# Kernel tuning notes

Hardware: AMD Instinct MI355X
Metric: run time of the kernel (lower is better)

The kernel has to match this reference:

```python
import jax, jax.numpy as jnp
import numpy as np

DIM = 512
NUM_HEADS = 8
HEAD_DIM = DIM // NUM_HEADS
SEGMENT_LENGTHS = (1024, 2048, 4096)
DILATED_RATIOS = (1, 2, 4)
SCALE = HEAD_DIM ** -0.5
NEG_FILL = -100000000.0  # matches torch masked_fill value


def setup_inputs() -> dict:
    key = jax.random.key(0)
    ks = jax.random.split(key, 8)
    b, L = 2, 8192
    def nrm(k, shape, s=1.0):
        return jax.random.normal(k, shape, dtype=jnp.float32) * s
    return {
        "query": nrm(ks[0], (b, L, DIM)),
        "key_": nrm(ks[1], (b, L, DIM)),
        "value": nrm(ks[2], (b, L, DIM)),
        "Wq": nrm(ks[3], (DIM, DIM), DIM ** -0.5),
        "Wk": nrm(ks[4], (DIM, DIM), DIM ** -0.5),
        "Wv": nrm(ks[5], (DIM, DIM), DIM ** -0.5),
        "Wo": nrm(ks[6], (DIM, DIM), DIM ** -0.5),
        "bo": nrm(ks[7], (DIM,), 0.01),
    }


def _branch(q, k, v, sl, dr):
    """One (segment_length, dilation) branch.
    q,k,v: (b, L, H, D). Returns dense out (b, L, H, D) and lse (b, L, H),
    with uncovered positions set to (0, NEG_FILL).
    gathering/dense_to_sparse reduces, per head hd, to selecting positions
    l*dr + (hd // (H//dr)) within each segment (diagonal of the r1 x r2 block).
    """
    b, L, H, D = q.shape
    n = L // sl          # segments per sequence
    hsub = H // dr       # heads per dilation offset
    lsub = sl // dr      # kept tokens per segment
    # (lsub, H): dilated position of each kept token for each head
    pos = jnp.arange(lsub)[:, None] * dr + (jnp.arange(H) // hsub)[None, :]
    hid = jnp.arange(H)[None, :]

    def gather(x):
        xs = x.reshape(b, n, sl, H, D)
        g = xs[:, :, pos, hid, :]                  # (b, n, lsub, H, D)
        return jnp.transpose(g, (0, 1, 3, 2, 4))    # (b, n, H, lsub, D)

    qi = gather(q) * SCALE
    ki = gather(k)
    vi = gather(v)
    scores = jnp.einsum('bnhld,bnhmd->bnhlm', qi, ki)
    lse = jax.nn.logsumexp(scores, axis=-1)                                  # (b, n, H, lsub)
    p = jax.nn.softmax(scores.astype(jnp.float32), axis=-1).astype(scores.dtype)
    o = jnp.einsum('bnhlm,bnhmd->bnhld', p, vi)                              # (b, n, H, lsub, D)
    # sparse_to_dense: scatter back onto dilated positions (diag_embed)
    o_ = jnp.transpose(o, (0, 1, 3, 2, 4))                                    # (b, n, lsub, H, D)
    od = jnp.zeros((b, n, sl, H, D), o.dtype).at[:, :, pos, hid, :].set(o_)
    ld = jnp.zeros((b, n, sl, H), lse.dtype).at[:, :, pos, hid].set(
        jnp.transpose(lse, (0, 1, 3, 2)))
    ld = jnp.where(ld == 0, NEG_FILL, ld)  # masked_fill_(lse == 0, -1e8)
    return od.reshape(b, L, H, D), ld.reshape(b, L, H)


def reference(query, key_, value, Wq, Wk, Wv, Wo, bo):
    b, L, _ = query.shape
    def heads(x, W):
        return (x @ W.T).reshape(b, L, NUM_HEADS, HEAD_DIM)
    q = heads(query, Wq)
    k = heads(key_, Wk)
    v = heads(value, Wv)
    outs, lses = [], []
    for sl, dr in zip(SEGMENT_LENGTHS, DILATED_RATIOS):
        o, l = _branch(q, k, v, sl, dr)
        outs.append(o)
        lses.append(l)
    # merge branches via logsumexp-weighted combination (weights detached in torch)
    lse_stack = jnp.stack(lses, 0)            # (nb, b, L, H)
    m = lse_stack.max(0)
    w = jnp.exp(lse_stack - m)
    w = w / w.sum(0)
    w = jax.lax.stop_gradient(w)
    out = sum(o * wi[..., None] for o, wi in zip(outs, list(w)))
    out = out.reshape(b, L, DIM)
    return out @ Wo.T + bo
```

## Files before the change

### kernel.cpp

```cpp
#include <hip/hip_runtime.h>
#include <hip/hip_bf16.h>

typedef unsigned short u16;
typedef unsigned int u32;
typedef __attribute__((ext_vector_type(8))) short short8;
typedef __attribute__((ext_vector_type(4))) float floatx4;
typedef __attribute__((ext_vector_type(2))) unsigned int uint2v;

__device__ __forceinline__ float b2f(u16 u) {
    u32 x = ((u32)u) << 16;
    return __builtin_bit_cast(float, x);
}
__device__ __forceinline__ u16 f2b(float f) {
    u32 x = __builtin_bit_cast(u32, f);
    return (u16)((x + 0x7fffu + ((x >> 16) & 1u)) >> 16);
}
__device__ __forceinline__ u32 pack2(float lo, float hi) {
    float2 f; f.x = lo; f.y = hi;
    __hip_bfloat162 h = __float22bfloat162_rn(f);
    u32 r;
    __builtin_memcpy(&r, &h, 4);
    return r;
}
__device__ __forceinline__ float fexp2(float x) {
#if __has_builtin(__builtin_amdgcn_exp2f)
    return __builtin_amdgcn_exp2f(x);
#else
    return __expf(x * 0.6931471805599453f);
#endif
}

__device__ __forceinline__ uint2v pl32(u32 a, u32 b) {
    return __builtin_amdgcn_permlane32_swap(a, b, false, false);
}

template<bool AF32>
__global__ __launch_bounds__(256) void gemm_bt_bias(
    const void* __restrict__ Ap, const float* __restrict__ B,
    u16* __restrict__ Cb, float* __restrict__ Cf, const float* __restrict__ bias,
    int M, int N, int K, float scale)
{
    __shared__ __align__(16) u16 a_lds[128][72];
    __shared__ __align__(16) u16 b_lds[128][72];
    const int tid = threadIdx.x;
    const int lane = tid & 63, wv = tid >> 6;
    const int quad = lane >> 4, l15 = lane & 15;
    const int tm = blockIdx.x, tn = blockIdx.y;
    const int wm = (wv >> 1) * 64, wn = (wv & 1) * 64;
    (void)M;

    floatx4 acc[4][4];
#pragma unroll
    for (int i = 0; i < 4; ++i)
#pragma unroll
        for (int j = 0; j < 4; ++j) acc[i][j] = (floatx4)0.f;

    for (int k0 = 0; k0 < K; k0 += 64) {
#pragma unroll
        for (int r = 0; r < 4; ++r) {
            int idx = r * 256 + tid;
            int row = idx >> 3, ch = (idx & 7) * 8;
            if constexpr (AF32) {
                const float* A = (const float*)Ap;
                const float* src = A + (size_t)(tm * 128 + row) * K + k0 + ch;
                float4 f0 = *(const float4*)src;
                float4 f1 = *(const float4*)(src + 4);
                uint4 pk;
                pk.x = pack2(f0.x, f0.y);
                pk.y = pack2(f0.z, f0.w);
                pk.z = pack2(f1.x, f1.y);
                pk.w = pack2(f1.z, f1.w);
                *(uint4*)&a_lds[row][ch] = pk;
            } else {
                const u16* A = (const u16*)Ap;
                *(uint4*)&a_lds[row][ch] =
                    *(const uint4*)(A + (size_t)(tm * 128 + row) * K + k0 + ch);
            }
            {
                const float* src = B + (size_t)(tn * 128 + row) * K + k0 + ch;
                float4 f0 = *(const float4*)src;
                float4 f1 = *(const float4*)(src + 4);
                uint4 pk;
                pk.x = pack2(f0.x, f0.y);
                pk.y = pack2(f0.z, f0.w);
                pk.z = pack2(f1.x, f1.y);
                pk.w = pack2(f1.z, f1.w);
                *(uint4*)&b_lds[row][ch] = pk;
            }
        }
        __syncthreads();
#pragma unroll
        for (int dc = 0; dc < 2; ++dc) {
            short8 af[4], bf[4];
#pragma unroll
            for (int mi = 0; mi < 4; ++mi)
                af[mi] = *(const short8*)&a_lds[wm + mi * 16 + l15][dc * 32 + quad * 8];
#pragma unroll
            for (int ni = 0; ni < 4; ++ni)
                bf[ni] = *(const short8*)&b_lds[wn + ni * 16 + l15][dc * 32 + quad * 8];
#pragma unroll
            for (int mi = 0; mi < 4; ++mi)
#pragma unroll
                for (int ni = 0; ni < 4; ++ni)
                    acc[mi][ni] = __builtin_amdgcn_mfma_f32_16x16x32_bf16(
                        af[mi], bf[ni], acc[mi][ni], 0, 0, 0);
        }
        __syncthreads();
    }
#pragma unroll
    for (int mi = 0; mi < 4; ++mi)
#pragma unroll
        for (int ni = 0; ni < 4; ++ni) {
            int col = tn * 128 + wn + ni * 16 + l15;
            float bb = bias ? bias[col] : 0.f;
#pragma unroll
            for (int r = 0; r < 4; ++r) {
                int row = tm * 128 + wm + mi * 16 + quad * 4 + r;
                float val = acc[mi][ni][r] * scale + bb;
                if (Cf) Cf[(size_t)row * N + col] = val;
                else    Cb[(size_t)row * N + col] = f2b(val);
            }
        }
}

__device__ __forceinline__ void decode_inst(int inst, int& b, int& s, int& h,
                                            int& sl, int& dr, int& phase)
{
    if (inst < 128)      { int j = inst;       b = j >> 6; s = (j >> 3) & 7; h = j & 7; sl = 1024; dr = 1; phase = 0;      }
    else if (inst < 192) { int j = inst - 128; b = j >> 5; s = (j >> 3) & 3; h = j & 7; sl = 2048; dr = 2; phase = h >> 2; }
    else                 { int j = inst - 192; b = j >> 4; s = (j >> 3) & 1; h = j & 7; sl = 4096; dr = 4; phase = h >> 1; }
}

__global__ __launch_bounds__(256) void gather_kv(
    const u16* __restrict__ kk, const u16* __restrict__ vv,
    u16* __restrict__ KG, u16* __restrict__ VT)
{
    int inst = blockIdx.x;
    int b, s, h, sl, dr, phase;
    decode_inst(inst, b, s, h, sl, dr, phase);
    int n0 = blockIdx.y * 32;
    __shared__ __align__(16) u16 tile[32][72];
    int tid = threadIdx.x;
    int row = tid >> 3, ch = (tid & 7) * 8;
    int n = n0 + row;
    size_t pos = (size_t)s * sl + (size_t)n * dr + phase;
    size_t src = (((size_t)b * 8192 + pos) * 8 + h) * 64 + ch;
    *(uint4*)(KG + ((size_t)inst * 1024 + n) * 64 + ch) = *(const uint4*)(kk + src);
    *(uint4*)&tile[row][ch] = *(const uint4*)(vv + src);
    __syncthreads();
    int d = tid >> 2, nn = (tid & 3) * 8;
    __align__(16) u16 tmp[8];
#pragma unroll
    for (int j = 0; j < 8; ++j) tmp[j] = tile[nn + j][d];
    *(uint4*)(VT + ((size_t)inst * 64 + d) * 1024 + n0 + nn) = *(uint4*)tmp;
}

__global__ __launch_bounds__(256, 4) void attn_kernel(
    const u16* __restrict__ q, const u16* __restrict__ KG,
    const u16* __restrict__ VT, u16* __restrict__ Og, float* __restrict__ Lg)
{
    const int inst = blockIdx.y, qt = blockIdx.x;
    int b, s, h, sl, dr, phase;
    decode_inst(inst, b, s, h, sl, dr, phase);
    __shared__ __align__(16) u16 k_lds[128][72];
    __shared__ __align__(16) u16 vt_lds[64][136];
    const int tid = threadIdx.x, lane = tid & 63, wv = tid >> 6;
    const int quad = lane >> 4, l15 = lane & 15;
    const int sl15 = (l15 & 3) | ((l15 & 4) << 1) | ((l15 & 8) >> 1);

    const int qrow = qt * 64 + wv * 16 + l15;
    const size_t qpos = (size_t)s * sl + (size_t)qrow * dr + phase;
    const u16* qbase = q + (((size_t)b * 8192 + qpos) * 8 + h) * 64;
    const short8 qf0 = *(const short8*)(qbase + quad * 8);
    const short8 qf1 = *(const short8*)(qbase + 32 + quad * 8);

    floatx4 oacc[4];
#pragma unroll
    for (int dt = 0; dt < 4; ++dt) oacc[dt] = (floatx4)0.f;
    float mst = -1e30f, lst = 0.f;

    const u16* KGb = KG + (size_t)inst * 65536;
    const u16* VTb = VT + (size_t)inst * 65536;

    for (int it = 0; it < 8; ++it) {
        const int k0 = it * 128;
#pragma unroll
        for (int r = 0; r < 4; ++r) {
            int idx = r * 256 + tid;
            int row = idx >> 3, ch = (idx & 7) * 8;
            *(uint4*)&k_lds[row][ch] =
                *(const uint4*)(KGb + (size_t)(k0 + row) * 64 + ch);
        }
#pragma unroll
        for (int r = 0; r < 4; ++r) {
            int idx = r * 256 + tid;
            int d = idx >> 4, ch = (idx & 15) * 8;
            *(uint4*)&vt_lds[d][ch] =
                *(const uint4*)(VTb + (size_t)d * 1024 + k0 + ch);
        }
        __syncthreads();

        floatx4 sacc[8];
#pragma unroll
        for (int nt = 0; nt < 8; ++nt) {
            sacc[nt] = (floatx4)0.f;
            short8 kf0 = *(const short8*)&k_lds[nt * 16 + sl15][quad * 8];
            short8 kf1 = *(const short8*)&k_lds[nt * 16 + sl15][32 + quad * 8];
            sacc[nt] = __builtin_amdgcn_mfma_f32_16x16x32_bf16(kf0, qf0, sacc[nt], 0, 0, 0);
            sacc[nt] = __builtin_amdgcn_mfma_f32_16x16x32_bf16(kf1, qf1, sacc[nt], 0, 0, 0);
        }

        float mx = sacc[0][0];
#pragma unroll
        for (int nt = 0; nt < 8; ++nt)
#pragma unroll
            for (int r = 0; r < 4; ++r) mx = fmaxf(mx, sacc[nt][r]);
        mx = fmaxf(mx, __shfl_xor(mx, 16, 64));
        mx = fmaxf(mx, __shfl_xor(mx, 32, 64));
        float mnew = fmaxf(mst, mx);
        float alpha = fexp2(mst - mnew);
        float rs = 0.f;
#pragma unroll
        for (int nt = 0; nt < 8; ++nt)
#pragma unroll
            for (int r = 0; r < 4; ++r) {
                float p = fexp2(sacc[nt][r] - mnew);
                sacc[nt][r] = p;
                rs += p;
            }
        rs += __shfl_xor(rs, 16, 64);
        rs += __shfl_xor(rs, 32, 64);
        lst = lst * alpha + rs;
        mst = mnew;
#pragma unroll
        for (int dt = 0; dt < 4; ++dt) oacc[dt] *= alpha;

#pragma unroll
        for (int nc = 0; nc < 4; ++nc) {
            u32 pk00 = pack2(sacc[2 * nc][0], sacc[2 * nc][1]);
            u32 pk01 = pack2(sacc[2 * nc][2], sacc[2 * nc][3]);
            u32 pk10 = pack2(sacc[2 * nc + 1][0], sacc[2 * nc + 1][1]);
            u32 pk11 = pack2(sacc[2 * nc + 1][2], sacc[2 * nc + 1][3]);
            uint2v xz = pl32(pk00, pk10);
            uint2v yw = pl32(pk01, pk11);
            uint4 bw;
            bw.x = xz[0];
            bw.y = yw[0];
            bw.z = xz[1];
            bw.w = yw[1];
            short8 pf = __builtin_bit_cast(short8, bw);
#pragma unroll
            for (int dt = 0; dt < 4; ++dt) {
                short8 vf = *(const short8*)&vt_lds[dt * 16 + l15][nc * 32 + quad * 8];
                oacc[dt] = __builtin_amdgcn_mfma_f32_16x16x32_bf16(vf, pf, oacc[dt], 0, 0, 0);
            }
        }
        __syncthreads();
    }

    float inv_l = (lst > 0.f) ? (1.f / lst) : 0.f;
#pragma unroll
    for (int dt = 0; dt < 4; ++dt) {
        u32 lo = pack2(oacc[dt][0] * inv_l, oacc[dt][1] * inv_l);
        u32 hi = pack2(oacc[dt][2] * inv_l, oacc[dt][3] * inv_l);
        uint2 v; v.x = lo; v.y = hi;
        *(uint2*)&k_lds[wv * 16 + l15][dt * 16 + quad * 4] = v;
    }
    __syncthreads();
#pragma unroll
    for (int c = 0; c < 2; ++c) {
        uint4 val = *(const uint4*)&k_lds[wv * 16 + l15][quad * 16 + c * 8];
        *(uint4*)(Og + (((size_t)inst * 1024 + qt * 64 + wv * 16 + l15) * 64
                        + quad * 16 + c * 8)) = val;
    }
    if (quad == 0) {
        Lg[(size_t)inst * 1024 + qt * 64 + wv * 16 + l15] = mst + __log2f(lst);
    }
}

__global__ __launch_bounds__(256) void merge_kernel(
    const u16* __restrict__ Og, const float* __restrict__ Lg,
    u16* __restrict__ merged)
{
    int bid = blockIdx.x;
    int b = bid >> 13, l = bid & 8191;
    int t = threadIdx.x;
    int h = t >> 5, d0 = (t & 31) * 2;

    int inst0 = b * 64 + ((l >> 10) << 3) + h;
    int row0 = l & 1023;
    int p1 = l & 2047;
    bool c1 = ((p1 & 1) == (h >> 2));
    int inst1 = 128 + b * 32 + ((l >> 11) << 3) + h;
    int row1 = p1 >> 1;
    int p2 = l & 4095;
    bool c2 = ((p2 & 3) == (h >> 1));
    int inst2 = 192 + b * 16 + ((l >> 12) << 3) + h;
    int row2 = p2 >> 2;

    float lse0 = Lg[(size_t)inst0 * 1024 + row0];
    float lse1 = c1 ? Lg[(size_t)inst1 * 1024 + row1] : -1e30f;
    float lse2 = c2 ? Lg[(size_t)inst2 * 1024 + row2] : -1e30f;
    float m = fmaxf(lse0, fmaxf(lse1, lse2));
    float w0 = fexp2(lse0 - m);
    float w1 = c1 ? fexp2(lse1 - m) : 0.f;
    float w2 = c2 ? fexp2(lse2 - m) : 0.f;
    float inv = 1.f / (w0 + w1 + w2);
    w0 *= inv; w1 *= inv; w2 *= inv;

    u32 u0 = *(const u32*)(Og + ((size_t)inst0 * 1024 + row0) * 64 + d0);
    u32 u1 = c1 ? *(const u32*)(Og + ((size_t)inst1 * 1024 + row1) * 64 + d0) : 0u;
    u32 u2 = c2 ? *(const u32*)(Og + ((size_t)inst2 * 1024 + row2) * 64 + d0) : 0u;
    float a0 = b2f((u16)(u0 & 0xffff)), e0 = b2f((u16)(u0 >> 16));
    float a1 = b2f((u16)(u1 & 0xffff)), e1 = b2f((u16)(u1 >> 16));
    float a2 = b2f((u16)(u2 & 0xffff)), e2 = b2f((u16)(u2 >> 16));
    float ra = w0 * a0 + w1 * a1 + w2 * a2;
    float rb = w0 * e0 + w1 * e1 + w2 * e2;
    u32 outp = pack2(ra, rb);
    *(u32*)(merged + (((size_t)b * 8192 + l) * 8 + h) * 64 + d0) = outp;
}

extern "C" void kernel_launch(void* const* d_in, const int* in_sizes, int n_in,
                              void* d_out, int out_size, void* d_ws, size_t ws_size,
                              hipStream_t stream)
{
    (void)in_sizes; (void)n_in; (void)out_size; (void)ws_size;
    const float* query = (const float*)d_in[0];
    const float* key_  = (const float*)d_in[1];
    const float* value = (const float*)d_in[2];
    const float* Wq    = (const float*)d_in[3];
    const float* Wk    = (const float*)d_in[4];
    const float* Wv    = (const float*)d_in[5];
    const float* Wo    = (const float*)d_in[6];
    const float* bo    = (const float*)d_in[7];

    char* ws = (char*)d_ws;
    const size_t SZ_PROJ = (size_t)16384 * 512 * 2;
    const size_t SZ_KG   = (size_t)224 * 1024 * 64 * 2;
    const size_t SZ_LG   = (size_t)224 * 1024 * 4;
    u16*   qb     = (u16*)(ws);
    u16*   kb     = (u16*)(ws + SZ_PROJ);
    u16*   vb     = (u16*)(ws + 2 * SZ_PROJ);
    u16*   KG     = (u16*)(ws + 3 * SZ_PROJ);
    u16*   VT     = (u16*)(ws + 3 * SZ_PROJ + SZ_KG);
    u16*   Og     = (u16*)(ws + 3 * SZ_PROJ + 2 * SZ_KG);
    float* Lg     = (float*)(ws + 3 * SZ_PROJ + 3 * SZ_KG);
    u16*   merged = (u16*)(ws + 3 * SZ_PROJ + 3 * SZ_KG + SZ_LG);

    const int M = 16384, N = 512, K = 512;
    const float SCALE = 0.125f * 1.44269504088896f;

    gemm_bt_bias<true><<<dim3(128, 4), 256, 0, stream>>>(query, Wq, qb, nullptr, nullptr, M, N, K, SCALE);
    gemm_bt_bias<true><<<dim3(128, 4), 256, 0, stream>>>(key_,  Wk, kb, nullptr, nullptr, M, N, K, 1.0f);
    gemm_bt_bias<true><<<dim3(128, 4), 256, 0, stream>>>(value, Wv, vb, nullptr, nullptr, M, N, K, 1.0f);
    gather_kv<<<dim3(224, 32), 256, 0, stream>>>(kb, vb, KG, VT);
    attn_kernel<<<dim3(16, 224), 256, 0, stream>>>(qb, KG, VT, Og, Lg);
    merge_kernel<<<16384, 256, 0, stream>>>(Og, Lg, merged);
    gemm_bt_bias<false><<<dim3(128, 4), 256, 0, stream>>>(merged, Wo, nullptr, (float*)d_out, bo, M, N, K, 1.0f);
}
```

Before: 388.8 us.

## Load attention K/V tiles via direct global-to-LDS loads with XOR-swizzled layout

The attention kernel now fills its K and V^T shared-memory tiles with global_load_lds instructions that write straight into LDS, bypassing registers. Because those loads cannot pad rows, the padded LDS arrays are replaced by unpadded ones, and the gather kernel pre-applies an XOR swizzle to the KG/VT layouts so that LDS reads stay bank-conflict free. The epilogue staging uses the same swizzle. This aims to cut VGPR traffic and instruction count in the load path, but it couples the gather and attention layouts and relies on the builtin's per-lane addressing being correct.

```diff
diff --git a/kernel.cpp b/kernel.cpp
--- a/kernel.cpp
+++ b/kernel.cpp
@@ -32,6 +32,12 @@
 
 __device__ __forceinline__ uint2v pl32(u32 a, u32 b) {
     return __builtin_amdgcn_permlane32_swap(a, b, false, false);
+}
+
+__device__ __forceinline__ void gl16(const u16* g, u16* l) {
+    __builtin_amdgcn_global_load_lds(
+        (const __attribute__((address_space(1))) void*)g,
+        (__attribute__((address_space(3))) void*)l, 16, 0, 0);
 }
 
 template<bool AF32>
@@ -145,14 +151,16 @@
     int n = n0 + row;
     size_t pos = (size_t)s * sl + (size_t)n * dr + phase;
     size_t src = (((size_t)b * 8192 + pos) * 8 + h) * 64 + ch;
-    *(uint4*)(KG + ((size_t)inst * 1024 + n) * 64 + ch) = *(const uint4*)(kk + src);
+    int chs = ch ^ ((n & 7) * 8);
+    *(uint4*)(KG + ((size_t)inst * 1024 + n) * 64 + chs) = *(const uint4*)(kk + src);
     *(uint4*)&tile[row][ch] = *(const uint4*)(vv + src);
     __syncthreads();
     int d = tid >> 2, nn = (tid & 3) * 8;
     __align__(16) u16 tmp[8];
 #pragma unroll
     for (int j = 0; j < 8; ++j) tmp[j] = tile[nn + j][d];
-    *(uint4*)(VT + ((size_t)inst * 64 + d) * 1024 + n0 + nn) = *(uint4*)tmp;
+    int col = (n0 + nn) ^ ((d & 7) * 8);
+    *(uint4*)(VT + ((size_t)inst * 64 + d) * 1024 + col) = *(uint4*)tmp;
 }
 
 __global__ __launch_bounds__(256, 4) void attn_kernel(
@@ -162,11 +170,13 @@
     const int inst = blockIdx.y, qt = blockIdx.x;
     int b, s, h, sl, dr, phase;
     decode_inst(inst, b, s, h, sl, dr, phase);
-    __shared__ __align__(16) u16 k_lds[128][72];
-    __shared__ __align__(16) u16 vt_lds[64][136];
+    __shared__ __align__(16) u16 k_lds[128][64];
+    __shared__ __align__(16) u16 vt_lds[64][128];
     const int tid = threadIdx.x, lane = tid & 63, wv = tid >> 6;
     const int quad = lane >> 4, l15 = lane & 15;
     const int sl15 = (l15 & 3) | ((l15 & 4) << 1) | ((l15 & 8) >> 1);
+    const int ksw = (sl15 & 7) * 8;
+    const int vsw = (l15 & 7) * 8;
 
     const int qrow = qt * 64 + wv * 16 + l15;
     const size_t qpos = (size_t)s * sl + (size_t)qrow * dr + phase;
@@ -181,22 +191,17 @@
 
     const u16* KGb = KG + (size_t)inst * 65536;
     const u16* VTb = VT + (size_t)inst * 65536;
+    u16* klb = &k_lds[0][0];
+    u16* vlb = &vt_lds[0][0];
 
     for (int it = 0; it < 8; ++it) {
         const int k0 = it * 128;
 #pragma unroll
         for (int r = 0; r < 4; ++r) {
-            int idx = r * 256 + tid;
-            int row = idx >> 3, ch = (idx & 7) * 8;
-            *(uint4*)&k_lds[row][ch] =
-                *(const uint4*)(KGb + (size_t)(k0 + row) * 64 + ch);
-        }
-#pragma unroll
-        for (int r = 0; r < 4; ++r) {
-            int idx = r * 256 + tid;
-            int d = idx >> 4, ch = (idx & 15) * 8;
-            *(uint4*)&vt_lds[d][ch] =
-                *(const uint4*)(VTb + (size_t)d * 1024 + k0 + ch);
+            int c = wv * 4 + r;
+            gl16(KGb + (size_t)k0 * 64 + c * 512 + lane * 8, klb + c * 512);
+            gl16(VTb + (size_t)(c * 4 + (lane >> 4)) * 1024 + k0 + (lane & 15) * 8,
+                 vlb + c * 512);
         }
         __syncthreads();
 
@@ -204,8 +209,8 @@
 #pragma unroll
         for (int nt = 0; nt < 8; ++nt) {
             sacc[nt] = (floatx4)0.f;
-            short8 kf0 = *(const short8*)&k_lds[nt * 16 + sl15][quad * 8];
-            short8 kf1 = *(const short8*)&k_lds[nt * 16 + sl15][32 + quad * 8];
+            short8 kf0 = *(const short8*)&k_lds[nt * 16 + sl15][(quad * 8) ^ ksw];
+            short8 kf1 = *(const short8*)&k_lds[nt * 16 + sl15][(32 + quad * 8) ^ ksw];
             sacc[nt] = __builtin_amdgcn_mfma_f32_16x16x32_bf16(kf0, qf0, sacc[nt], 0, 0, 0);
             sacc[nt] = __builtin_amdgcn_mfma_f32_16x16x32_bf16(kf1, qf1, sacc[nt], 0, 0, 0);
         }
@@ -251,25 +256,27 @@
             short8 pf = __builtin_bit_cast(short8, bw);
 #pragma unroll
             for (int dt = 0; dt < 4; ++dt) {
-                short8 vf = *(const short8*)&vt_lds[dt * 16 + l15][nc * 32 + quad * 8];
+                short8 vf = *(const short8*)
+                    &vt_lds[dt * 16 + l15][(nc * 32 + quad * 8) ^ vsw];
                 oacc[dt] = __builtin_amdgcn_mfma_f32_16x16x32_bf16(vf, pf, oacc[dt], 0, 0, 0);
             }
         }
         __syncthreads();
     }
 
+    const int esw = (l15 & 7) * 8;
     float inv_l = (lst > 0.f) ? (1.f / lst) : 0.f;
 #pragma unroll
     for (int dt = 0; dt < 4; ++dt) {
         u32 lo = pack2(oacc[dt][0] * inv_l, oacc[dt][1] * inv_l);
         u32 hi = pack2(oacc[dt][2] * inv_l, oacc[dt][3] * inv_l);
         uint2 v; v.x = lo; v.y = hi;
-        *(uint2*)&k_lds[wv * 16 + l15][dt * 16 + quad * 4] = v;
+        *(uint2*)&k_lds[wv * 16 + l15][(dt * 16 + quad * 4) ^ esw] = v;
     }
     __syncthreads();
 #pragma unroll
     for (int c = 0; c < 2; ++c) {
-        uint4 val = *(const uint4*)&k_lds[wv * 16 + l15][quad * 16 + c * 8];
+        uint4 val = *(const uint4*)&k_lds[wv * 16 + l15][(quad * 16 + c * 8) ^ esw];
         *(uint4*)(Og + (((size_t)inst * 1024 + qt * 64 + wv * 16 + l15) * 64
                         + quad * 16 + c * 8)) = val;
     }
```

Result: faster. 353.1 us (-9.2%).
